# Kernel tuning notes

Measured on AMD Instinct MI355X. Metric: run time of the kernel, lower is better.

## Reference

```python
import jax, jax.numpy as jnp
import numpy as np

N = 50000
IN_DIM = 128
HID = 128
HEADS = 4
NEG_SLOPE = 0.2


def setup_inputs() -> dict:
    key = jax.random.key(0)
    ks = jax.random.split(key, 12)
    x = jax.random.normal(ks[0], (N, IN_DIM), dtype=jnp.float32)
    edge_index = jax.random.randint(ks[1], (2, 800000), 0, N, dtype=jnp.int64)
    s = 0.05
    # layer 1: in -> heads*hid, concat
    W1 = jax.random.normal(ks[2], (IN_DIM, HEADS * HID), dtype=jnp.float32) * s
    a_src1 = jax.random.normal(ks[3], (HEADS, HID), dtype=jnp.float32) * s
    a_dst1 = jax.random.normal(ks[4], (HEADS, HID), dtype=jnp.float32) * s
    b1 = jnp.zeros((HEADS * HID,), dtype=jnp.float32)
    # layer 2: heads*hid -> hid, 1 head
    W2 = jax.random.normal(ks[5], (HEADS * HID, HID), dtype=jnp.float32) * s
    a_src2 = jax.random.normal(ks[6], (1, HID), dtype=jnp.float32) * s
    a_dst2 = jax.random.normal(ks[7], (1, HID), dtype=jnp.float32) * s
    b2 = jnp.zeros((HID,), dtype=jnp.float32)
    fc_w = jax.random.normal(ks[8], (HID, 1), dtype=jnp.float32) * s
    fc_b = jnp.zeros((1,), dtype=jnp.float32)
    return {"x": x, "edge_index": edge_index, "W1": W1, "a_src1": a_src1,
            "a_dst1": a_dst1, "b1": b1, "W2": W2, "a_src2": a_src2,
            "a_dst2": a_dst2, "b2": b2, "fc_w": fc_w, "fc_b": fc_b}


def gat_conv(x, src, dst, W, a_src, a_dst, b, heads, ch):
    n = x.shape[0]
    xh = (x @ W).reshape(n, heads, ch)                      # [N,H,C]
    alpha_s = jnp.einsum('nhc,hc->nh', xh, a_src)           # [N,H]
    alpha_d = jnp.einsum('nhc,hc->nh', xh, a_dst)           # [N,H]
    e = alpha_s[src] + alpha_d[dst]                         # [E,H]
    e = jnp.where(e > 0, e, NEG_SLOPE * e)                  # LeakyReLU(0.2)
    # segment softmax over edges grouped by destination node
    m = jax.ops.segment_max(e, dst, num_segments=n)         # [N,H]
    ex = jnp.exp(e - m[dst])
    denom = jax.ops.segment_sum(ex, dst, num_segments=n)    # [N,H]
    alpha = ex / denom[dst]                                 # [E,H]
    msg = xh[src] * alpha[:, :, None]                       # [E,H,C]
    out = jax.ops.segment_sum(msg, dst, num_segments=n)     # [N,H,C]
    return out.reshape(n, heads * ch) + b


def reference(x, edge_index, W1, a_src1, a_dst1, b1, W2, a_src2, a_dst2, b2, fc_w, fc_b):
    n = x.shape[0]
    loop = jnp.arange(n, dtype=edge_index.dtype)
    src = jnp.concatenate([edge_index[0], loop])            # PyG add_self_loops=True
    dst = jnp.concatenate([edge_index[1], loop])
    h = gat_conv(x, src, dst, W1, a_src1, a_dst1, b1, HEADS, HID)
    h = jax.nn.elu(h)  # dropout is identity in eval mode
    h = gat_conv(h, src, dst, W2, a_src2, a_dst2, b2, 1, HID)
    return (h @ fc_w + fc_b).squeeze(-1)                    # [N]
```

## Files before the change

kernel.cpp:

```cpp
#include <hip/hip_runtime.h>

#define IN_DIM 128

typedef unsigned int u32;
typedef unsigned short u16;
typedef __attribute__((ext_vector_type(8))) short bf16x8;
typedef __attribute__((ext_vector_type(4))) float f32x4;
typedef __attribute__((ext_vector_type(4))) u32 u32x4;

__device__ __forceinline__ float bf2f(u32 b) { return __uint_as_float(b << 16); }
__device__ __forceinline__ u16 f2bf(float f) {
  u32 u = __float_as_uint(f);
  u += 0x7fffu + ((u >> 16) & 1u);
  return (u16)(u >> 16);
}
__device__ __forceinline__ u32 pk2(float a, float b) {
  return (u32)f2bf(a) | ((u32)f2bf(b) << 16);
}

__global__ void k_init(const u32* __restrict__ ei, int* __restrict__ hdr, int* __restrict__ cnt,
                       const float* __restrict__ W1, const float* __restrict__ as1v,
                       const float* __restrict__ ad1v, const float* __restrict__ W2,
                       const float* __restrict__ as2v, const float* __restrict__ ad2v,
                       const float* __restrict__ b2, const float* __restrict__ fcw,
                       const float* __restrict__ fcb,
                       float* __restrict__ w1s, float* __restrict__ w1d,
                       float* __restrict__ w2s, float* __restrict__ w2d,
                       float* __restrict__ fc2, float* __restrict__ cbuf,
                       u16* __restrict__ wt1, int E, int N, int nzb) {
  const int b = blockIdx.x;
  if (b < nzb) {
    int t = b * 256 + threadIdx.x;
    if (t < N) cnt[t] = 0;
    if (t == 0) {
      int i64 = 1;
      int kmax = (2 * E < 257) ? 2 * E : 257;
      for (int k = 1; k < kmax; k += 2) i64 &= (ei[k] == 0u);
      hdr[0] = i64;
      hdr[1] = 0;
    }
    if (t < 512) {
      int h = t >> 7, k = t & 127;
      float s = 0.f;
      for (int c = 0; c < 128; ++c) s = fmaf(W1[(size_t)k * 512 + h * 128 + c], as1v[h * 128 + c], s);
      w1s[t] = s;
    } else if (t < 1024) {
      int j = t - 512;
      int h = j >> 7, k = j & 127;
      float s = 0.f;
      for (int c = 0; c < 128; ++c) s = fmaf(W1[(size_t)k * 512 + h * 128 + c], ad1v[h * 128 + c], s);
      w1d[j] = s;
    } else if (t < 1536) {
      int k = t - 1024;
      float s = 0.f;
      for (int c = 0; c < 128; ++c) s = fmaf(W2[(size_t)k * 128 + c], as2v[c], s);
      w2s[k] = s;
    } else if (t < 2048) {
      int k = t - 1536;
      float s = 0.f;
      for (int c = 0; c < 128; ++c) s = fmaf(W2[(size_t)k * 128 + c], ad2v[c], s);
      w2d[k] = s;
    } else if (t < 2560) {
      int k = t - 2048;
      float s = 0.f;
      for (int c = 0; c < 128; ++c) s = fmaf(W2[(size_t)k * 128 + c], fcw[c], s);
      fc2[k] = s;
    } else if (t == 2560) {
      float s = 0.f;
      for (int c = 0; c < 128; ++c) s = fmaf(b2[c], fcw[c], s);
      cbuf[0] = s + fcb[0];
    }
  } else {
    int j = (b - nzb) * 256 + threadIdx.x;
    int n = j >> 7, k = j & 127;
    wt1[j] = f2bf(W1[(size_t)k * 512 + n]);
  }
}

__global__ void k_convprep(const void* __restrict__ ei, int* __restrict__ src32,
                           int* __restrict__ dst32, int* __restrict__ rank,
                           int* __restrict__ cnt,
                           const float* __restrict__ x, u16* __restrict__ xbf,
                           const float* __restrict__ w1s, const float* __restrict__ w1d,
                           float* __restrict__ as1, float* __restrict__ ad1,
                           int E, int gE4, int N, const int* __restrict__ eflag) {
  const int b = blockIdx.x;
  if (b < gE4) {
    const int i0 = (b * 256 + threadIdx.x) * 4;
    if (i0 >= E) return;
    if (i0 + 3 < E) {
      int s0, s1, s2, s3, d0, d1, d2, d3;
      if (*eflag) {
        const long long* p = (const long long*)ei;
        const int4 aa = *(const int4*)(p + i0);
        const int4 ab = *(const int4*)(p + i0 + 2);
        const int4 ba = *(const int4*)(p + E + i0);
        const int4 bb = *(const int4*)(p + E + i0 + 2);
        s0 = aa.x; s1 = aa.z; s2 = ab.x; s3 = ab.z;
        d0 = ba.x; d1 = ba.z; d2 = bb.x; d3 = bb.z;
      } else {
        const int* p = (const int*)ei;
        const int4 sv = *(const int4*)(p + i0);
        const int4 dv = *(const int4*)(p + E + i0);
        s0 = sv.x; s1 = sv.y; s2 = sv.z; s3 = sv.w;
        d0 = dv.x; d1 = dv.y; d2 = dv.z; d3 = dv.w;
      }
      const int r0 = atomicAdd(&cnt[d0], 1);
      const int r1 = atomicAdd(&cnt[d1], 1);
      const int r2 = atomicAdd(&cnt[d2], 1);
      const int r3 = atomicAdd(&cnt[d3], 1);
      int4 t;
      t.x = s0; t.y = s1; t.z = s2; t.w = s3; *(int4*)(src32 + i0) = t;
      t.x = d0; t.y = d1; t.z = d2; t.w = d3; *(int4*)(dst32 + i0) = t;
      t.x = r0; t.y = r1; t.z = r2; t.w = r3; *(int4*)(rank + i0) = t;
    } else {
      for (int i = i0; i < E; ++i) {
        int s, d;
        if (*eflag) {
          const long long* p = (const long long*)ei;
          s = (int)p[i]; d = (int)p[E + i];
        } else {
          const int* p = (const int*)ei;
          s = p[i]; d = p[E + i];
        }
        src32[i] = s; dst32[i] = d;
        rank[i] = atomicAdd(&cnt[d], 1);
      }
    }
  } else {
    const int wv = threadIdx.x >> 6, lane = threadIdx.x & 63;
    const int q = (b - gE4) * 16 + wv * 4 + (lane >> 4);
    const int sl = lane & 15;
    if (q >= N) return;
    const float4 xa = *(const float4*)(x + (size_t)q * 128 + sl * 8);
    const float4 xb = *(const float4*)(x + (size_t)q * 128 + sl * 8 + 4);
    u32x4 pk = {pk2(xa.x, xa.y), pk2(xa.z, xa.w), pk2(xb.x, xb.y), pk2(xb.z, xb.w)};
    *(u32x4*)(xbf + (size_t)q * 128 + sl * 8) = pk;
    float p[8];
    #pragma unroll
    for (int h = 0; h < 4; ++h) {
      const float4 wa = *(const float4*)(w1s + h * 128 + sl * 8);
      const float4 wb = *(const float4*)(w1s + h * 128 + sl * 8 + 4);
      p[h] = xa.x * wa.x + xa.y * wa.y + xa.z * wa.z + xa.w * wa.w +
             xb.x * wb.x + xb.y * wb.y + xb.z * wb.z + xb.w * wb.w;
      const float4 va = *(const float4*)(w1d + h * 128 + sl * 8);
      const float4 vb = *(const float4*)(w1d + h * 128 + sl * 8 + 4);
      p[4 + h] = xa.x * va.x + xa.y * va.y + xa.z * va.z + xa.w * va.w +
                 xb.x * vb.x + xb.y * vb.y + xb.z * vb.z + xb.w * vb.w;
    }
    #pragma unroll
    for (int s = 8; s; s >>= 1)
      #pragma unroll
      for (int k = 0; k < 8; ++k) p[k] += __shfl_xor(p[k], s);
    if (sl == 0) {
      float4 vs = {p[0], p[1], p[2], p[3]};
      float4 vd = {p[4], p[5], p[6], p[7]};
      ((float4*)as1)[q] = vs;
      ((float4*)ad1)[q] = vd;
    }
  }
}

__global__ void k_alloc(const int* __restrict__ cnt, int* __restrict__ rowp,
                        int* __restrict__ total, int N) {
  int i = blockIdx.x * blockDim.x + threadIdx.x;
  int lane = threadIdx.x & 63;
  int v = (i < N) ? cnt[i] + 1 : 0;
  int s = v;
  #pragma unroll
  for (int off = 1; off < 64; off <<= 1) {
    int t = __shfl_up(s, off);
    if (lane >= off) s += t;
  }
  int waveTotal = __shfl(s, 63);
  int base = 0;
  if (lane == 63) base = atomicAdd(total, waveTotal);
  base = __shfl(base, 63);
  int r = base + s - v;
  if (i < N) rowp[i] = r;
}

__global__ void k_scatter(const int* __restrict__ src32, const int* __restrict__ dst32,
                          const int* __restrict__ rank, const int* __restrict__ rowp,
                          const int* __restrict__ cnt, int* __restrict__ csr,
                          int E4, int E, int N) {
  int t = blockIdx.x * blockDim.x + threadIdx.x;
  if (t < E4) {
    const int i0 = t * 4;
    if (i0 + 3 < E) {
      const int4 s4 = *(const int4*)(src32 + i0);
      const int4 d4 = *(const int4*)(dst32 + i0);
      const int4 r4 = *(const int4*)(rank + i0);
      csr[rowp[d4.x] + r4.x] = s4.x;
      csr[rowp[d4.y] + r4.y] = s4.y;
      csr[rowp[d4.z] + r4.z] = s4.z;
      csr[rowp[d4.w] + r4.w] = s4.w;
    } else {
      for (int i = i0; i < E; ++i) csr[rowp[dst32[i]] + rank[i]] = src32[i];
    }
  } else {
    const int n = t - E4;
    if (n < N) csr[rowp[n] + cnt[n]] = n;
  }
}

#define CAP1 128
__global__ __launch_bounds__(256) void k_agg1(
    const u16* __restrict__ xbf, const float* __restrict__ as_, const float* __restrict__ ad_,
    const int* __restrict__ csr, const int* __restrict__ rowp, const int* __restrict__ cnt,
    u16* __restrict__ aggx, int N) {
  __shared__ int s_src[4][CAP1];
  __shared__ float s_ex[4][CAP1][4];
  const int wv = threadIdx.x >> 6, lane = threadIdx.x & 63;
  const int dn = blockIdx.x * 4 + wv;
  if (dn >= N) return;
  const int start = rowp[dn], deg = cnt[dn] + 1;
  const float4 ad4 = *(const float4*)(ad_ + (size_t)dn * 4);
  float d0 = 0.f, d1 = 0.f, d2 = 0.f, d3 = 0.f;
  float acc[4][2] = {};
  for (int c0 = 0; c0 < deg; c0 += CAP1) {
    const int cn = min(CAP1, deg - c0);
    for (int i = lane; i < cn; i += 64) {
      const int s = csr[start + c0 + i];
      s_src[wv][i] = s;
      const float4 a4 = *(const float4*)(as_ + (size_t)s * 4);
      float e, ex;
      e = a4.x + ad4.x; e = e > 0.f ? e : 0.2f * e; ex = __expf(e); s_ex[wv][i][0] = ex; d0 += ex;
      e = a4.y + ad4.y; e = e > 0.f ? e : 0.2f * e; ex = __expf(e); s_ex[wv][i][1] = ex; d1 += ex;
      e = a4.z + ad4.z; e = e > 0.f ? e : 0.2f * e; ex = __expf(e); s_ex[wv][i][2] = ex; d2 += ex;
      e = a4.w + ad4.w; e = e > 0.f ? e : 0.2f * e; ex = __expf(e); s_ex[wv][i][3] = ex; d3 += ex;
    }
    int i = 0;
    for (; i + 1 < cn; i += 2) {
      const u32 w0 = ((const u32*)xbf)[(size_t)s_src[wv][i] * 64 + lane];
      const u32 w1 = ((const u32*)xbf)[(size_t)s_src[wv][i + 1] * 64 + lane];
      const float4 e0 = *(const float4*)(s_ex[wv][i]);
      const float4 e1 = *(const float4*)(s_ex[wv][i + 1]);
      const float x00 = bf2f(w0 & 0xffffu), x01 = __uint_as_float(w0 & 0xffff0000u);
      const float x10 = bf2f(w1 & 0xffffu), x11 = __uint_as_float(w1 & 0xffff0000u);
      acc[0][0] = fmaf(e0.x, x00, acc[0][0]); acc[0][1] = fmaf(e0.x, x01, acc[0][1]);
      acc[1][0] = fmaf(e0.y, x00, acc[1][0]); acc[1][1] = fmaf(e0.y, x01, acc[1][1]);
      acc[2][0] = fmaf(e0.z, x00, acc[2][0]); acc[2][1] = fmaf(e0.z, x01, acc[2][1]);
      acc[3][0] = fmaf(e0.w, x00, acc[3][0]); acc[3][1] = fmaf(e0.w, x01, acc[3][1]);
      acc[0][0] = fmaf(e1.x, x10, acc[0][0]); acc[0][1] = fmaf(e1.x, x11, acc[0][1]);
      acc[1][0] = fmaf(e1.y, x10, acc[1][0]); acc[1][1] = fmaf(e1.y, x11, acc[1][1]);
      acc[2][0] = fmaf(e1.z, x10, acc[2][0]); acc[2][1] = fmaf(e1.z, x11, acc[2][1]);
      acc[3][0] = fmaf(e1.w, x10, acc[3][0]); acc[3][1] = fmaf(e1.w, x11, acc[3][1]);
    }
    if (i < cn) {
      const u32 w0 = ((const u32*)xbf)[(size_t)s_src[wv][i] * 64 + lane];
      const float4 e0 = *(const float4*)(s_ex[wv][i]);
      const float x00 = bf2f(w0 & 0xffffu), x01 = __uint_as_float(w0 & 0xffff0000u);
      acc[0][0] = fmaf(e0.x, x00, acc[0][0]); acc[0][1] = fmaf(e0.x, x01, acc[0][1]);
      acc[1][0] = fmaf(e0.y, x00, acc[1][0]); acc[1][1] = fmaf(e0.y, x01, acc[1][1]);
      acc[2][0] = fmaf(e0.z, x00, acc[2][0]); acc[2][1] = fmaf(e0.z, x01, acc[2][1]);
      acc[3][0] = fmaf(e0.w, x00, acc[3][0]); acc[3][1] = fmaf(e0.w, x01, acc[3][1]);
    }
  }
  #pragma unroll
  for (int s = 32; s; s >>= 1) {
    d0 += __shfl_xor(d0, s); d1 += __shfl_xor(d1, s);
    d2 += __shfl_xor(d2, s); d3 += __shfl_xor(d3, s);
  }
  const float i0 = 1.f / d0, i1 = 1.f / d1, i2 = 1.f / d2, i3 = 1.f / d3;
  u32* orow = (u32*)aggx + (size_t)dn * 256 + lane;
  orow[0]   = pk2(acc[0][0] * i0, acc[0][1] * i0);
  orow[64]  = pk2(acc[1][0] * i1, acc[1][1] * i1);
  orow[128] = pk2(acc[2][0] * i2, acc[2][1] * i2);
  orow[192] = pk2(acc[3][0] * i3, acc[3][1] * i3);
}

#define SWZ(row, blk) ((((blk) ^ ((row) & 15))) * 8)

__global__ __launch_bounds__(256) void k_mm(const u16* __restrict__ A, const u16* __restrict__ BT,
                                            const float* __restrict__ bias,
                                            const float* __restrict__ wS, const float* __restrict__ wD,
                                            const float* __restrict__ wZ,
                                            float* __restrict__ asO, float* __restrict__ adO,
                                            float* __restrict__ zO, int M) {
  __shared__ u16 As[128 * 128];
  __shared__ u16 Bs[128 * 128];
  __shared__ float red[128][4];
  const int tid = threadIdx.x;
  const int wid = tid >> 6, lane = tid & 63;
  const int wr = wid >> 1, wc = wid & 1;
  const int m0 = blockIdx.x * 128;
  const int fr = lane & 15, g4 = lane >> 4;
  const int col = lane & 15, rbase = (lane >> 4) * 4;
  float ps[4][4] = {}, pd[4][4] = {}, pz[4][4] = {};
  for (int h = 0; h < 4; ++h) {
    #pragma unroll
    for (int j = 0; j < 8; ++j) {
      const int g = j * 256 + tid;
      const int row = g >> 4, blk = g & 15;
      const int gm = m0 + row;
      const uint4 z = {0, 0, 0, 0};
      const uint4 va = (gm < M) ? *(const uint4*)(A + (size_t)gm * 512 + h * 128 + blk * 8) : z;
      const uint4 vb = *(const uint4*)(BT + (size_t)(h * 128 + row) * 128 + blk * 8);
      *(uint4*)(&As[row * 128 + SWZ(row, blk)]) = va;
      *(uint4*)(&Bs[row * 128 + SWZ(row, blk)]) = vb;
    }
    __syncthreads();
    float bws[4], bwd[4], bwz[4];
    f32x4 acc[4][4];
    #pragma unroll
    for (int n = 0; n < 4; ++n) {
      const int gn = h * 128 + wc * 64 + n * 16 + col;
      const float bb = bias[gn];
      bws[n] = wS[gn]; bwd[n] = wD[gn]; bwz[n] = wZ[gn];
      const f32x4 bi = {bb, bb, bb, bb};
      #pragma unroll
      for (int m = 0; m < 4; ++m) acc[m][n] = bi;
    }
    #pragma unroll
    for (int ks = 0; ks < 4; ++ks) {
      bf16x8 af[4], bfr[4];
      #pragma unroll
      for (int m = 0; m < 4; ++m) {
        const int R = wr * 64 + m * 16 + fr;
        af[m] = *(const bf16x8*)(&As[R * 128 + SWZ(R, ks * 4 + g4)]);
      }
      #pragma unroll
      for (int n = 0; n < 4; ++n) {
        const int R = wc * 64 + n * 16 + fr;
        bfr[n] = *(const bf16x8*)(&Bs[R * 128 + SWZ(R, ks * 4 + g4)]);
      }
      #pragma unroll
      for (int m = 0; m < 4; ++m)
        #pragma unroll
        for (int n = 0; n < 4; ++n)
          acc[m][n] = __builtin_amdgcn_mfma_f32_16x16x32_bf16(af[m], bfr[n], acc[m][n], 0, 0, 0);
    }
    #pragma unroll
    for (int m = 0; m < 4; ++m)
      #pragma unroll
      for (int q = 0; q < 4; ++q) {
        float s = 0.f, d = 0.f, zz = 0.f;
        #pragma unroll
        for (int n = 0; n < 4; ++n) {
          float v = acc[m][n][q];
          v = v > 0.f ? v : __expf(v) - 1.f;
          s = fmaf(v, bws[n], s);
          d = fmaf(v, bwd[n], d);
          zz = fmaf(v, bwz[n], zz);
        }
        ps[m][q] += s; pd[m][q] += d; pz[m][q] += zz;
      }
    __syncthreads();
  }
  #pragma unroll
  for (int sh = 1; sh < 16; sh <<= 1)
    #pragma unroll
    for (int m = 0; m < 4; ++m)
      #pragma unroll
      for (int q = 0; q < 4; ++q) {
        ps[m][q] += __shfl_xor(ps[m][q], sh);
        pd[m][q] += __shfl_xor(pd[m][q], sh);
        pz[m][q] += __shfl_xor(pz[m][q], sh);
      }
  if (col == 0 && wc == 1) {
    #pragma unroll
    for (int m = 0; m < 4; ++m)
      #pragma unroll
      for (int q = 0; q < 4; ++q) {
        const int r = wr * 64 + m * 16 + rbase + q;
        red[r][0] = ps[m][q]; red[r][1] = pd[m][q]; red[r][2] = pz[m][q];
      }
  }
  __syncthreads();
  if (col == 0 && wc == 0) {
    #pragma unroll
    for (int m = 0; m < 4; ++m)
      #pragma unroll
      for (int q = 0; q < 4; ++q) {
        const int r = wr * 64 + m * 16 + rbase + q;
        const int gm = m0 + r;
        if (gm < M) {
          asO[gm] = ps[m][q] + red[r][0];
          adO[gm] = pd[m][q] + red[r][1];
          zO[gm]  = pz[m][q] + red[r][2];
        }
      }
  }
}

__global__ __launch_bounds__(256) void k_agg2(
    const float* __restrict__ as_, const float* __restrict__ ad_, const float* __restrict__ z,
    const int* __restrict__ csr, const int* __restrict__ rowp, const int* __restrict__ cnt,
    const float* __restrict__ cbuf, float* __restrict__ out, int N) {
  const int grp = threadIdx.x >> 4, gl = threadIdx.x & 15;
  const int dn = blockIdx.x * 16 + grp;
  if (dn >= N) return;
  const int start = rowp[dn], deg = cnt[dn] + 1;
  const float adv = ad_[dn];
  float dsum = 0.f, zsum = 0.f;
  for (int i = gl; i < deg; i += 16) {
    const int s = csr[start + i];
    float e = as_[s] + adv;
    e = e > 0.f ? e : 0.2f * e;
    const float ex = __expf(e);
    dsum += ex;
    zsum = fmaf(ex, z[s], zsum);
  }
  #pragma unroll
  for (int s = 8; s; s >>= 1) {
    dsum += __shfl_xor(dsum, s);
    zsum += __shfl_xor(zsum, s);
  }
  if (gl == 0) out[dn] = zsum / dsum + cbuf[0];
}

extern "C" void kernel_launch(void* const* d_in, const int* in_sizes, int n_in,
                              void* d_out, int out_size, void* d_ws, size_t ws_size,
                              hipStream_t stream) {
  const float* x      = (const float*)d_in[0];
  const void*  ei     = d_in[1];
  const float* W1     = (const float*)d_in[2];
  const float* a_src1 = (const float*)d_in[3];
  const float* a_dst1 = (const float*)d_in[4];
  const float* b1     = (const float*)d_in[5];
  const float* W2     = (const float*)d_in[6];
  const float* a_src2 = (const float*)d_in[7];
  const float* a_dst2 = (const float*)d_in[8];
  const float* b2     = (const float*)d_in[9];
  const float* fc_w   = (const float*)d_in[10];
  const float* fc_b   = (const float*)d_in[11];
  const int N = in_sizes[0] / IN_DIM;
  const int E = in_sizes[1] / 2;

  char* w = (char*)d_ws;
  size_t off = 0;
  auto take = [&](size_t bytes) -> char* {
    char* p = w + off;
    off += (bytes + 255) & ~(size_t)255;
    return p;
  };
  int*   hdr    = (int*)take(256);
  int*   src32  = (int*)take((size_t)E * 4);
  int*   dst32  = (int*)take((size_t)E * 4);
  int*   rank   = (int*)take((size_t)E * 4);
  int*   cnt    = (int*)take((size_t)N * 4);
  int*   rowp   = (int*)take((size_t)N * 4);
  int*   csr    = (int*)take((size_t)(E + N) * 4);
  float* as1    = (float*)take((size_t)N * 16);
  float* ad1    = (float*)take((size_t)N * 16);
  float* as2    = (float*)take((size_t)N * 4);
  float* ad2    = (float*)take((size_t)N * 4);
  float* zv     = (float*)take((size_t)N * 4);
  float* w1s    = (float*)take(512 * 4);
  float* w1d    = (float*)take(512 * 4);
  float* w2s    = (float*)take(512 * 4);
  float* w2d    = (float*)take(512 * 4);
  float* fc2    = (float*)take(512 * 4);
  float* cbuf   = (float*)take(256);
  u16*   xbf    = (u16*)take((size_t)N * 128 * 2);
  u16*   wt1    = (u16*)take((size_t)512 * 128 * 2);
  u16*   aggx   = (u16*)take((size_t)N * 512 * 2);
  (void)ws_size; (void)n_in; (void)out_size;

  const int nzb = (N + 255) / 256;
  k_init<<<nzb + 256, 256, 0, stream>>>((const u32*)ei, hdr, cnt, W1, a_src1, a_dst1,
                                        W2, a_src2, a_dst2, b2, fc_w, fc_b,
                                        w1s, w1d, w2s, w2d, fc2, cbuf, wt1, E, N, nzb);

  const int gE4 = (E / 4 + 255) / 256 + ((E % 4) ? 1 : 0);
  const int gN16 = (N + 15) / 16;
  k_convprep<<<gE4 + gN16, 256, 0, stream>>>(ei, src32, dst32, rank, cnt, x, xbf,
                                             w1s, w1d, as1, ad1, E, gE4, N, hdr);
  k_alloc<<<(N + 255) / 256, 256, 0, stream>>>(cnt, rowp, hdr + 1, N);

  const int E4 = (E + 3) / 4;
  k_scatter<<<(E4 + N + 255) / 256, 256, 0, stream>>>(src32, dst32, rank, rowp, cnt, csr,
                                                      E4, E, N);

  k_agg1<<<(N + 3) / 4, 256, 0, stream>>>(xbf, as1, ad1, csr, rowp, cnt, aggx, N);

  const int mt = (N + 127) / 128;
  k_mm<<<mt, 256, 0, stream>>>(aggx, wt1, b1, w2s, w2d, fc2, as2, ad2, zv, N);

  k_agg2<<<(N + 15) / 16, 256, 0, stream>>>(as2, ad2, zv, csr, rowp, cnt, cbuf,
                                            (float*)d_out, N);
}
```

Before: 173.0 us.

## Use 16-bit edge indices, parallelize weight-prep GEMVs, tile W1 transpose, pack FMAs

Edge source, destination, rank and CSR arrays are stored as 16-bit values instead of 32-bit. This halves the index traffic in the scatter and both aggregation kernels, and it relies on N and node degrees staying below 65536. The small weight-folding GEMVs in the init kernel are spread across 16-lane groups with shuffle reductions instead of running as serial per-thread loops. The W1 bf16 transpose now goes through a shared-memory tile. The layer-1 aggregation accumulators use two-wide vector FMAs so the compiler can emit packed FP32 math.

```diff
diff --git a/kernel.cpp b/kernel.cpp
--- a/kernel.cpp
+++ b/kernel.cpp
@@ -6,6 +6,7 @@
 typedef unsigned short u16;
 typedef __attribute__((ext_vector_type(8))) short bf16x8;
 typedef __attribute__((ext_vector_type(4))) float f32x4;
+typedef __attribute__((ext_vector_type(2))) float f32x2;
 typedef __attribute__((ext_vector_type(4))) u32 u32x4;
 
 __device__ __forceinline__ float bf2f(u32 b) { return __uint_as_float(b << 16); }
@@ -18,67 +19,79 @@
   return (u32)f2bf(a) | ((u32)f2bf(b) << 16);
 }
 
+#define GEMV_BLOCKS 161
 __global__ void k_init(const u32* __restrict__ ei, int* __restrict__ hdr, int* __restrict__ cnt,
                        const float* __restrict__ W1, const float* __restrict__ as1v,
                        const float* __restrict__ ad1v, const float* __restrict__ W2,
                        const float* __restrict__ as2v, const float* __restrict__ ad2v,
-                       const float* __restrict__ b2, const float* __restrict__ fcw,
+                       const float* __restrict__ b2v, const float* __restrict__ fcw,
                        const float* __restrict__ fcb,
                        float* __restrict__ w1s, float* __restrict__ w1d,
                        float* __restrict__ w2s, float* __restrict__ w2d,
                        float* __restrict__ fc2, float* __restrict__ cbuf,
                        u16* __restrict__ wt1, int E, int N, int nzb) {
   const int b = blockIdx.x;
+  const int t = threadIdx.x;
   if (b < nzb) {
-    int t = b * 256 + threadIdx.x;
-    if (t < N) cnt[t] = 0;
-    if (t == 0) {
+    int i = b * 256 + t;
+    if (i < N) cnt[i] = 0;
+    if (b == 0 && t == 0) {
       int i64 = 1;
       int kmax = (2 * E < 257) ? 2 * E : 257;
       for (int k = 1; k < kmax; k += 2) i64 &= (ei[k] == 0u);
       hdr[0] = i64;
       hdr[1] = 0;
     }
-    if (t < 512) {
-      int h = t >> 7, k = t & 127;
-      float s = 0.f;
-      for (int c = 0; c < 128; ++c) s = fmaf(W1[(size_t)k * 512 + h * 128 + c], as1v[h * 128 + c], s);
-      w1s[t] = s;
-    } else if (t < 1024) {
-      int j = t - 512;
-      int h = j >> 7, k = j & 127;
-      float s = 0.f;
-      for (int c = 0; c < 128; ++c) s = fmaf(W1[(size_t)k * 512 + h * 128 + c], ad1v[h * 128 + c], s);
-      w1d[j] = s;
-    } else if (t < 1536) {
-      int k = t - 1024;
-      float s = 0.f;
-      for (int c = 0; c < 128; ++c) s = fmaf(W2[(size_t)k * 128 + c], as2v[c], s);
-      w2s[k] = s;
-    } else if (t < 2048) {
-      int k = t - 1536;
-      float s = 0.f;
-      for (int c = 0; c < 128; ++c) s = fmaf(W2[(size_t)k * 128 + c], ad2v[c], s);
-      w2d[k] = s;
-    } else if (t < 2560) {
-      int k = t - 2048;
-      float s = 0.f;
-      for (int c = 0; c < 128; ++c) s = fmaf(W2[(size_t)k * 128 + c], fcw[c], s);
-      fc2[k] = s;
-    } else if (t == 2560) {
-      float s = 0.f;
-      for (int c = 0; c < 128; ++c) s = fmaf(b2[c], fcw[c], s);
-      cbuf[0] = s + fcb[0];
-    }
+  } else if (b < nzb + GEMV_BLOCKS) {
+    const int o = (b - nzb) * 16 + (t >> 4);
+    const int gl = t & 15;
+    if (o > 2560) return;
+    const float* row;
+    const float* vec;
+    float* outp;
+    float extra = 0.f;
+    if (o < 512) {
+      const int h = o >> 7, k = o & 127;
+      row = W1 + (size_t)k * 512 + (h << 7); vec = as1v + (h << 7); outp = w1s + o;
+    } else if (o < 1024) {
+      const int j = o - 512, h = j >> 7, k = j & 127;
+      row = W1 + (size_t)k * 512 + (h << 7); vec = ad1v + (h << 7); outp = w1d + j;
+    } else if (o < 1536) {
+      const int k = o - 1024;
+      row = W2 + (size_t)k * 128; vec = as2v; outp = w2s + k;
+    } else if (o < 2048) {
+      const int k = o - 1536;
+      row = W2 + (size_t)k * 128; vec = ad2v; outp = w2d + k;
+    } else if (o < 2560) {
+      const int k = o - 2048;
+      row = W2 + (size_t)k * 128; vec = fcw; outp = fc2 + k;
+    } else {
+      row = b2v; vec = fcw; outp = cbuf; extra = fcb[0];
+    }
+    const float4 ra = ((const float4*)row)[gl * 2], rb = ((const float4*)row)[gl * 2 + 1];
+    const float4 va = ((const float4*)vec)[gl * 2], vb = ((const float4*)vec)[gl * 2 + 1];
+    float s = ra.x * va.x + ra.y * va.y + ra.z * va.z + ra.w * va.w +
+              rb.x * vb.x + rb.y * vb.y + rb.z * vb.z + rb.w * vb.w;
+    #pragma unroll
+    for (int m = 8; m; m >>= 1) s += __shfl_xor(s, m, 16);
+    if (gl == 0) *outp = s + extra;
   } else {
-    int j = (b - nzb) * 256 + threadIdx.x;
-    int n = j >> 7, k = j & 127;
-    wt1[j] = f2bf(W1[(size_t)k * 512 + n]);
-  }
-}
-
-__global__ void k_convprep(const void* __restrict__ ei, int* __restrict__ src32,
-                           int* __restrict__ dst32, int* __restrict__ rank,
+    __shared__ float tile[32][33];
+    const int b2 = b - nzb - GEMV_BLOCKS;
+    const int k0 = (b2 & 3) * 32, n0 = (b2 >> 2) * 32;
+    const int tx = t & 31, ty = t >> 5;
+    #pragma unroll
+    for (int p = 0; p < 4; ++p)
+      tile[ty + p * 8][tx] = W1[(size_t)(k0 + ty + p * 8) * 512 + n0 + tx];
+    __syncthreads();
+    #pragma unroll
+    for (int p = 0; p < 4; ++p)
+      wt1[(size_t)(n0 + ty + p * 8) * 128 + k0 + tx] = f2bf(tile[tx][ty + p * 8]);
+  }
+}
+
+__global__ void k_convprep(const void* __restrict__ ei, u16* __restrict__ src16,
+                           u16* __restrict__ dst16, u16* __restrict__ rank16,
                            int* __restrict__ cnt,
                            const float* __restrict__ x, u16* __restrict__ xbf,
                            const float* __restrict__ w1s, const float* __restrict__ w1d,
@@ -109,10 +122,13 @@
       const int r1 = atomicAdd(&cnt[d1], 1);
       const int r2 = atomicAdd(&cnt[d2], 1);
       const int r3 = atomicAdd(&cnt[d3], 1);
-      int4 t;
-      t.x = s0; t.y = s1; t.z = s2; t.w = s3; *(int4*)(src32 + i0) = t;
-      t.x = d0; t.y = d1; t.z = d2; t.w = d3; *(int4*)(dst32 + i0) = t;
-      t.x = r0; t.y = r1; t.z = r2; t.w = r3; *(int4*)(rank + i0) = t;
+      ushort4 t;
+      t.x = (u16)s0; t.y = (u16)s1; t.z = (u16)s2; t.w = (u16)s3;
+      *(ushort4*)(src16 + i0) = t;
+      t.x = (u16)d0; t.y = (u16)d1; t.z = (u16)d2; t.w = (u16)d3;
+      *(ushort4*)(dst16 + i0) = t;
+      t.x = (u16)r0; t.y = (u16)r1; t.z = (u16)r2; t.w = (u16)r3;
+      *(ushort4*)(rank16 + i0) = t;
     } else {
       for (int i = i0; i < E; ++i) {
         int s, d;
@@ -123,8 +139,8 @@
           const int* p = (const int*)ei;
           s = p[i]; d = p[E + i];
         }
-        src32[i] = s; dst32[i] = d;
-        rank[i] = atomicAdd(&cnt[d], 1);
+        src16[i] = (u16)s; dst16[i] = (u16)d;
+        rank16[i] = (u16)atomicAdd(&cnt[d], 1);
       }
     }
   } else {
@@ -151,7 +167,7 @@
     #pragma unroll
     for (int s = 8; s; s >>= 1)
       #pragma unroll
-      for (int k = 0; k < 8; ++k) p[k] += __shfl_xor(p[k], s);
+      for (int k = 0; k < 8; ++k) p[k] += __shfl_xor(p[k], s, 16);
     if (sl == 0) {
       float4 vs = {p[0], p[1], p[2], p[3]};
       float4 vd = {p[4], p[5], p[6], p[7]};
@@ -180,34 +196,34 @@
   if (i < N) rowp[i] = r;
 }
 
-__global__ void k_scatter(const int* __restrict__ src32, const int* __restrict__ dst32,
-                          const int* __restrict__ rank, const int* __restrict__ rowp,
-                          const int* __restrict__ cnt, int* __restrict__ csr,
+__global__ void k_scatter(const u16* __restrict__ src16, const u16* __restrict__ dst16,
+                          const u16* __restrict__ rank16, const int* __restrict__ rowp,
+                          const int* __restrict__ cnt, u16* __restrict__ csr,
                           int E4, int E, int N) {
   int t = blockIdx.x * blockDim.x + threadIdx.x;
   if (t < E4) {
     const int i0 = t * 4;
     if (i0 + 3 < E) {
-      const int4 s4 = *(const int4*)(src32 + i0);
-      const int4 d4 = *(const int4*)(dst32 + i0);
-      const int4 r4 = *(const int4*)(rank + i0);
+      const ushort4 s4 = *(const ushort4*)(src16 + i0);
+      const ushort4 d4 = *(const ushort4*)(dst16 + i0);
+      const ushort4 r4 = *(const ushort4*)(rank16 + i0);
       csr[rowp[d4.x] + r4.x] = s4.x;
       csr[rowp[d4.y] + r4.y] = s4.y;
       csr[rowp[d4.z] + r4.z] = s4.z;
       csr[rowp[d4.w] + r4.w] = s4.w;
     } else {
-      for (int i = i0; i < E; ++i) csr[rowp[dst32[i]] + rank[i]] = src32[i];
+      for (int i = i0; i < E; ++i) csr[rowp[dst16[i]] + rank16[i]] = src16[i];
     }
   } else {
     const int n = t - E4;
-    if (n < N) csr[rowp[n] + cnt[n]] = n;
+    if (n < N) csr[rowp[n] + cnt[n]] = (u16)n;
   }
 }
 
 #define CAP1 128
 __global__ __launch_bounds__(256) void k_agg1(
     const u16* __restrict__ xbf, const float* __restrict__ as_, const float* __restrict__ ad_,
-    const int* __restrict__ csr, const int* __restrict__ rowp, const int* __restrict__ cnt,
+    const u16* __restrict__ csr, const int* __restrict__ rowp, const int* __restrict__ cnt,
     u16* __restrict__ aggx, int N) {
   __shared__ int s_src[4][CAP1];
   __shared__ float s_ex[4][CAP1][4];
@@ -217,7 +233,7 @@
   const int start = rowp[dn], deg = cnt[dn] + 1;
   const float4 ad4 = *(const float4*)(ad_ + (size_t)dn * 4);
   float d0 = 0.f, d1 = 0.f, d2 = 0.f, d3 = 0.f;
-  float acc[4][2] = {};
+  f32x2 acc[4] = {};
   for (int c0 = 0; c0 < deg; c0 += CAP1) {
     const int cn = min(CAP1, deg - c0);
     for (int i = lane; i < cn; i += 64) {
@@ -236,25 +252,25 @@
       const u32 w1 = ((const u32*)xbf)[(size_t)s_src[wv][i + 1] * 64 + lane];
       const float4 e0 = *(const float4*)(s_ex[wv][i]);
       const float4 e1 = *(const float4*)(s_ex[wv][i + 1]);
-      const float x00 = bf2f(w0 & 0xffffu), x01 = __uint_as_float(w0 & 0xffff0000u);
-      const float x10 = bf2f(w1 & 0xffffu), x11 = __uint_as_float(w1 & 0xffff0000u);
-      acc[0][0] = fmaf(e0.x, x00, acc[0][0]); acc[0][1] = fmaf(e0.x, x01, acc[0][1]);
-      acc[1][0] = fmaf(e0.y, x00, acc[1][0]); acc[1][1] = fmaf(e0.y, x01, acc[1][1]);
-      acc[2][0] = fmaf(e0.z, x00, acc[2][0]); acc[2][1] = fmaf(e0.z, x01, acc[2][1]);
-      acc[3][0] = fmaf(e0.w, x00, acc[3][0]); acc[3][1] = fmaf(e0.w, x01, acc[3][1]);
-      acc[0][0] = fmaf(e1.x, x10, acc[0][0]); acc[0][1] = fmaf(e1.x, x11, acc[0][1]);
-      acc[1][0] = fmaf(e1.y, x10, acc[1][0]); acc[1][1] = fmaf(e1.y, x11, acc[1][1]);
-      acc[2][0] = fmaf(e1.z, x10, acc[2][0]); acc[2][1] = fmaf(e1.z, x11, acc[2][1]);
-      acc[3][0] = fmaf(e1.w, x10, acc[3][0]); acc[3][1] = fmaf(e1.w, x11, acc[3][1]);
+      const f32x2 x0 = {bf2f(w0 & 0xffffu), __uint_as_float(w0 & 0xffff0000u)};
+      const f32x2 x1 = {bf2f(w1 & 0xffffu), __uint_as_float(w1 & 0xffff0000u)};
+      acc[0] = __builtin_elementwise_fma((f32x2){e0.x, e0.x}, x0, acc[0]);
+      acc[1] = __builtin_elementwise_fma((f32x2){e0.y, e0.y}, x0, acc[1]);
+      acc[2] = __builtin_elementwise_fma((f32x2){e0.z, e0.z}, x0, acc[2]);
+      acc[3] = __builtin_elementwise_fma((f32x2){e0.w, e0.w}, x0, acc[3]);
+      acc[0] = __builtin_elementwise_fma((f32x2){e1.x, e1.x}, x1, acc[0]);
+      acc[1] = __builtin_elementwise_fma((f32x2){e1.y, e1.y}, x1, acc[1]);
+      acc[2] = __builtin_elementwise_fma((f32x2){e1.z, e1.z}, x1, acc[2]);
+      acc[3] = __builtin_elementwise_fma((f32x2){e1.w, e1.w}, x1, acc[3]);
     }
     if (i < cn) {
       const u32 w0 = ((const u32*)xbf)[(size_t)s_src[wv][i] * 64 + lane];
       const float4 e0 = *(const float4*)(s_ex[wv][i]);
-      const float x00 = bf2f(w0 & 0xffffu), x01 = __uint_as_float(w0 & 0xffff0000u);
-      acc[0][0] = fmaf(e0.x, x00, acc[0][0]); acc[0][1] = fmaf(e0.x, x01, acc[0][1]);
-      acc[1][0] = fmaf(e0.y, x00, acc[1][0]); acc[1][1] = fmaf(e0.y, x01, acc[1][1]);
-      acc[2][0] = fmaf(e0.z, x00, acc[2][0]); acc[2][1] = fmaf(e0.z, x01, acc[2][1]);
-      acc[3][0] = fmaf(e0.w, x00, acc[3][0]); acc[3][1] = fmaf(e0.w, x01, acc[3][1]);
+      const f32x2 x0 = {bf2f(w0 & 0xffffu), __uint_as_float(w0 & 0xffff0000u)};
+      acc[0] = __builtin_elementwise_fma((f32x2){e0.x, e0.x}, x0, acc[0]);
+      acc[1] = __builtin_elementwise_fma((f32x2){e0.y, e0.y}, x0, acc[1]);
+      acc[2] = __builtin_elementwise_fma((f32x2){e0.z, e0.z}, x0, acc[2]);
+      acc[3] = __builtin_elementwise_fma((f32x2){e0.w, e0.w}, x0, acc[3]);
     }
   }
   #pragma unroll
@@ -264,10 +280,10 @@
   }
   const float i0 = 1.f / d0, i1 = 1.f / d1, i2 = 1.f / d2, i3 = 1.f / d3;
   u32* orow = (u32*)aggx + (size_t)dn * 256 + lane;
-  orow[0]   = pk2(acc[0][0] * i0, acc[0][1] * i0);
-  orow[64]  = pk2(acc[1][0] * i1, acc[1][1] * i1);
-  orow[128] = pk2(acc[2][0] * i2, acc[2][1] * i2);
-  orow[192] = pk2(acc[3][0] * i3, acc[3][1] * i3);
+  orow[0]   = pk2(acc[0].x * i0, acc[0].y * i0);
+  orow[64]  = pk2(acc[1].x * i1, acc[1].y * i1);
+  orow[128] = pk2(acc[2].x * i2, acc[2].y * i2);
+  orow[192] = pk2(acc[3].x * i3, acc[3].y * i3);
 }
 
 #define SWZ(row, blk) ((((blk) ^ ((row) & 15))) * 8)
@@ -386,7 +402,7 @@
 
 __global__ __launch_bounds__(256) void k_agg2(
     const float* __restrict__ as_, const float* __restrict__ ad_, const float* __restrict__ z,
-    const int* __restrict__ csr, const int* __restrict__ rowp, const int* __restrict__ cnt,
+    const u16* __restrict__ csr, const int* __restrict__ rowp, const int* __restrict__ cnt,
     const float* __restrict__ cbuf, float* __restrict__ out, int N) {
   const int grp = threadIdx.x >> 4, gl = threadIdx.x & 15;
   const int dn = blockIdx.x * 16 + grp;
@@ -436,12 +452,12 @@
     return p;
   };
   int*   hdr    = (int*)take(256);
-  int*   src32  = (int*)take((size_t)E * 4);
-  int*   dst32  = (int*)take((size_t)E * 4);
-  int*   rank   = (int*)take((size_t)E * 4);
+  u16*   src16  = (u16*)take((size_t)E * 2);
+  u16*   dst16  = (u16*)take((size_t)E * 2);
+  u16*   rank16 = (u16*)take((size_t)E * 2);
   int*   cnt    = (int*)take((size_t)N * 4);
   int*   rowp   = (int*)take((size_t)N * 4);
-  int*   csr    = (int*)take((size_t)(E + N) * 4);
+  u16*   csr    = (u16*)take((size_t)(E + N) * 2);
   float* as1    = (float*)take((size_t)N * 16);
   float* ad1    = (float*)take((size_t)N * 16);
   float* as2    = (float*)take((size_t)N * 4);
@@ -459,18 +475,18 @@
   (void)ws_size; (void)n_in; (void)out_size;
 
   const int nzb = (N + 255) / 256;
-  k_init<<<nzb + 256, 256, 0, stream>>>((const u32*)ei, hdr, cnt, W1, a_src1, a_dst1,
-                                        W2, a_src2, a_dst2, b2, fc_w, fc_b,
-                                        w1s, w1d, w2s, w2d, fc2, cbuf, wt1, E, N, nzb);
+  k_init<<<nzb + GEMV_BLOCKS + 64, 256, 0, stream>>>(
+      (const u32*)ei, hdr, cnt, W1, a_src1, a_dst1, W2, a_src2, a_dst2, b2, fc_w, fc_b,
+      w1s, w1d, w2s, w2d, fc2, cbuf, wt1, E, N, nzb);
 
   const int gE4 = (E / 4 + 255) / 256 + ((E % 4) ? 1 : 0);
   const int gN16 = (N + 15) / 16;
-  k_convprep<<<gE4 + gN16, 256, 0, stream>>>(ei, src32, dst32, rank, cnt, x, xbf,
+  k_convprep<<<gE4 + gN16, 256, 0, stream>>>(ei, src16, dst16, rank16, cnt, x, xbf,
                                              w1s, w1d, as1, ad1, E, gE4, N, hdr);
   k_alloc<<<(N + 255) / 256, 256, 0, stream>>>(cnt, rowp, hdr + 1, N);
 
   const int E4 = (E + 3) / 4;
-  k_scatter<<<(E4 + N + 255) / 256, 256, 0, stream>>>(src32, dst32, rank, rowp, cnt, csr,
+  k_scatter<<<(E4 + N + 255) / 256, 256, 0, stream>>>(src16, dst16, rank16, rowp, cnt, csr,
                                                       E4, E, N);
 
   k_agg1<<<(N + 3) / 4, 256, 0, stream>>>(xbf, as1, ad1, csr, rowp, cnt, aggx, N);
```

Result: faster. 168.4 us (-2.6%).
